# Optimization experiments

Measured on AMD Instinct MI355X. Metric: run time of the kernel, lower is better.

## Reference

```python
import jax, jax.numpy as jnp
import numpy as np

N = 4_194_304      # rows
B = 64             # buckets
KB = 20            # base hinge knots
KA = 20            # adjustment hinge knots


def setup_inputs() -> dict:
    key = jax.random.key(0)
    k_x, k_bi, k_wb, k_bb, k_wa, k_ba = jax.random.split(key, 6)
    x = jax.random.uniform(k_x, (N, 1), dtype=jnp.float32)
    bucket_idx = jax.random.randint(k_bi, (N,), 0, B, dtype=jnp.int32)
    # base hinge: knots over global [x_lo, x_hi] = [0, 1]
    base_knots = jnp.linspace(0.0, 1.0, KB, dtype=jnp.float32)
    base_w = jax.random.normal(k_wb, (KB,), dtype=jnp.float32) * 0.1
    base_b = jax.random.normal(k_bb, (), dtype=jnp.float32) * 0.1
    # per-bucket adjustment hinges: knots over each bucket's [x_min, x_max] = [0, 1]
    adj_knots = jnp.broadcast_to(jnp.linspace(0.0, 1.0, KA, dtype=jnp.float32), (B, KA))
    adj_w = jax.random.normal(k_wa, (B, KA), dtype=jnp.float32) * 0.05
    adj_b = jax.random.normal(k_ba, (B,), dtype=jnp.float32) * 0.05
    return {"x": x, "bucket_idx": bucket_idx, "base_knots": base_knots,
            "base_w": base_w, "base_b": base_b, "adj_knots": adj_knots,
            "adj_w": adj_w, "adj_b": adj_b}


def reference(x, bucket_idx, base_knots, base_w, base_b, adj_knots, adj_w, adj_b):
    # x: [N,1], bucket_idx: [N]
    xf = x[:, 0]                                            # [N]
    # shared base hinge: bias + sum_k w_k * relu(x - t_k)
    base = jnp.einsum('nk,k->n', jax.nn.relu(xf[:, None] - base_knots), base_w) + base_b
    # per-bucket adjustment hinge, fused gather (no per-bucket loop):
    kb = adj_knots[bucket_idx]                              # [N,KA]
    wb = adj_w[bucket_idx]                                  # [N,KA]
    adj = jnp.sum(jax.nn.relu(xf[:, None] - kb) * wb, axis=-1) + adj_b[bucket_idx]
    return (base + adj)[:, None]                            # [N,1]
```

## Files before the change

### kernel.cpp

```cpp
#include <hip/hip_runtime.h>


#define NBUCK 64
#define NKNOT 20

__device__ __forceinline__ float eval_one(float xf, int b, const float2* tab) {
    int j = (int)(xf * (float)(NKNOT - 1));
    j = j < 0 ? 0 : (j > NKNOT - 1 ? NKNOT - 1 : j);
    float2 st = tab[b * NKNOT + j];
    return fmaf(xf, st.x, -st.y);
}

__global__ __launch_bounds__(256) void bah_kernel(
    const float* __restrict__ x,
    const int*   __restrict__ bidx,
    const float* __restrict__ base_knots,
    const float* __restrict__ base_w,
    const float* __restrict__ base_b,
    const float* __restrict__ adj_knots,
    const float* __restrict__ adj_w,
    const float* __restrict__ adj_b,
    float* __restrict__ out,
    int n)
{
    __shared__ float2 tab[NBUCK * NKNOT];

    int t = threadIdx.x;
    if (t < NBUCK) {
        float c = base_b[0] + adj_b[t];
        float S = 0.0f, T = 0.0f;
        #pragma unroll
        for (int j = 0; j < NKNOT; ++j) {
            float wb = base_w[j];
            float wa = adj_w[t * NKNOT + j];
            S += wb + wa;
            T = fmaf(wb, base_knots[j], T);
            T = fmaf(wa, adj_knots[t * NKNOT + j], T);
            tab[t * NKNOT + j] = make_float2(S, T - c);
        }
    }
    __syncthreads();

    int n4 = n >> 2;
    const float4* x4 = (const float4*)x;
    const int4*   b4 = (const int4*)bidx;
    float4*       o4 = (float4*)out;
    int stride = gridDim.x * blockDim.x;

    for (int i = blockIdx.x * blockDim.x + threadIdx.x; i < n4; i += stride) {
        float4 xv = x4[i];
        int4   bv = b4[i];
        float4 ov;
        ov.x = eval_one(xv.x, bv.x, tab);
        ov.y = eval_one(xv.y, bv.y, tab);
        ov.z = eval_one(xv.z, bv.z, tab);
        ov.w = eval_one(xv.w, bv.w, tab);
        o4[i] = ov;
    }

    int tail_start = n4 << 2;
    for (int i = tail_start + blockIdx.x * blockDim.x + threadIdx.x; i < n;
         i += stride) {
        out[i] = eval_one(x[i], bidx[i], tab);
    }
}

extern "C" void kernel_launch(void* const* d_in, const int* in_sizes, int n_in,
                              void* d_out, int out_size, void* d_ws, size_t ws_size,
                              hipStream_t stream) {
    const float* x          = (const float*)d_in[0];
    const int*   bidx       = (const int*)d_in[1];
    const float* base_knots = (const float*)d_in[2];
    const float* base_w     = (const float*)d_in[3];
    const float* base_b     = (const float*)d_in[4];
    const float* adj_knots  = (const float*)d_in[5];
    const float* adj_w      = (const float*)d_in[6];
    const float* adj_b      = (const float*)d_in[7];
    float*       out        = (float*)d_out;

    int n = in_sizes[0];
    int threads = 256;
    int blocks  = 1024;

    bah_kernel<<<blocks, threads, 0, stream>>>(
        x, bidx, base_knots, base_w, base_b, adj_knots, adj_w, adj_b, out, n);
}
```

Before: 91.55 us.

## Replace grid-stride loop with two hoisted loads per thread and nontemporal stores

The grid-stride loop becomes a fixed two-item-per-thread body. Both items' x and bucket loads are issued before any compute, and results are written with nontemporal stores. The grid doubles to 2048 blocks and launch bounds add an occupancy hint. The goal is more memory-level parallelism and less cache pollution from the output stream. The cost is that every block now rebuilds the shared lookup table, so that setup runs twice as many times. The vector part also covers only 2*grid*block float4 items, so larger inputs would be silently incomplete.

```diff
diff --git a/kernel.cpp b/kernel.cpp
--- a/kernel.cpp
+++ b/kernel.cpp
@@ -3,6 +3,8 @@
 
 #define NBUCK 64
 #define NKNOT 20
+
+typedef float v4f __attribute__((ext_vector_type(4)));
 
 __device__ __forceinline__ float eval_one(float xf, int b, const float2* tab) {
     int j = (int)(xf * (float)(NKNOT - 1));
@@ -11,7 +13,7 @@
     return fmaf(xf, st.x, -st.y);
 }
 
-__global__ __launch_bounds__(256) void bah_kernel(
+__global__ __launch_bounds__(256, 8) void bah_kernel(
     const float* __restrict__ x,
     const int*   __restrict__ bidx,
     const float* __restrict__ base_knots,
@@ -41,26 +43,40 @@
     }
     __syncthreads();
 
-    int n4 = n >> 2;
+    int n4     = n >> 2;
+    int tid    = blockIdx.x * blockDim.x + threadIdx.x;
+    int stride = gridDim.x * blockDim.x;
     const float4* x4 = (const float4*)x;
     const int4*   b4 = (const int4*)bidx;
-    float4*       o4 = (float4*)out;
-    int stride = gridDim.x * blockDim.x;
+    v4f*          o4 = (v4f*)out;
 
-    for (int i = blockIdx.x * blockDim.x + threadIdx.x; i < n4; i += stride) {
-        float4 xv = x4[i];
-        int4   bv = b4[i];
-        float4 ov;
-        ov.x = eval_one(xv.x, bv.x, tab);
-        ov.y = eval_one(xv.y, bv.y, tab);
-        ov.z = eval_one(xv.z, bv.z, tab);
-        ov.w = eval_one(xv.w, bv.w, tab);
-        o4[i] = ov;
+    int i0 = tid, i1 = tid + stride;
+    bool v0 = i0 < n4, v1 = i1 < n4;
+
+    float4 xa, xb;
+    int4   ba, bb;
+    if (v0) { xa = x4[i0]; ba = b4[i0]; }
+    if (v1) { xb = x4[i1]; bb = b4[i1]; }
+
+    if (v0) {
+        v4f ov;
+        ov.x = eval_one(xa.x, ba.x, tab);
+        ov.y = eval_one(xa.y, ba.y, tab);
+        ov.z = eval_one(xa.z, ba.z, tab);
+        ov.w = eval_one(xa.w, ba.w, tab);
+        __builtin_nontemporal_store(ov, &o4[i0]);
+    }
+    if (v1) {
+        v4f ov;
+        ov.x = eval_one(xb.x, bb.x, tab);
+        ov.y = eval_one(xb.y, bb.y, tab);
+        ov.z = eval_one(xb.z, bb.z, tab);
+        ov.w = eval_one(xb.w, bb.w, tab);
+        __builtin_nontemporal_store(ov, &o4[i1]);
     }
 
-    int tail_start = n4 << 2;
-    for (int i = tail_start + blockIdx.x * blockDim.x + threadIdx.x; i < n;
-         i += stride) {
+    int tail_start = (n4 << 2);
+    for (int i = tail_start + tid; i < n; i += 2 * stride) {
         out[i] = eval_one(x[i], bidx[i], tab);
     }
 }
@@ -80,7 +96,7 @@
 
     int n = in_sizes[0];
     int threads = 256;
-    int blocks  = 1024;
+    int blocks  = 2048;
 
     bah_kernel<<<blocks, threads, 0, stream>>>(
         x, bidx, base_knots, base_w, base_b, adj_knots, adj_w, adj_b, out, n);
```

Measured after the change: 90.67 us. About the same (-1.0%).
